# Kernel tuning notes

Measured on AMD Instinct MI355X. Metric: run time of the kernel, lower is better.

The kernel has to match this reference:

```python
import jax, jax.numpy as jnp
import numpy as np

VOCAB = 32000
DEMBED = 512


def embed_position(dembed):
    # Faithful to the torch code: ep[1::2] = ep[0::2]; ep = 1/10000**(ep/dembed);
    # pos = arange(dembed) * ep; odd -> cos, even -> sin.
    i = jnp.arange(dembed, dtype=jnp.float32)
    ep_idx = jnp.floor(i / 2.0) * 2.0           # even index duplicated to the following odd slot
    ep = 1.0 / jnp.power(10000.0, ep_idx / dembed)
    pos = i * ep
    is_odd = (jnp.arange(dembed) % 2) == 1
    return jnp.where(is_odd, jnp.cos(pos), jnp.sin(pos))  # [dembed]


def setup_inputs() -> dict:
    key = jax.random.key(0)
    k1, k2 = jax.random.split(key)
    x = jax.random.randint(k1, (64, 1024), 0, VOCAB, dtype=jnp.int64)
    table = jax.random.normal(k2, (VOCAB, DEMBED), dtype=jnp.float32)
    return {"x": x, "table": table}


def reference(x, table):
    # one-hot matmul == direct gather; fuse with positional add
    pos = embed_position(table.shape[1])         # [dembed]
    return table[x] + pos                        # [B, S, dembed]
```

## Files before the change

kernel.cpp:

```cpp
#include <hip/hip_runtime.h>
#include <hip/hip_bf16.h>
#include <math.h>

#define DEMBED 512
#define NTOK   (64 * 1024)
#define TPB    256
#define BLOCKS 2048
#define STRIDE (BLOCKS * TPB)
#define N4     (NTOK * (DEMBED / 4))
#define ITERS  (N4 / STRIDE)

typedef float f4 __attribute__((ext_vector_type(4)));

__global__ void __launch_bounds__(TPB)
embed_kernel(const int* __restrict__ x,
             const float* __restrict__ table,
             float* __restrict__ out)
{
    const int tid = blockIdx.x * TPB + threadIdx.x;
    const int d4  = tid & 127;

    f4 p;
    const float kLog = logf(10000.0f) / (float)DEMBED;
#pragma unroll
    for (int j = 0; j < 4; ++j) {
        int   i      = d4 * 4 + j;
        float ep_idx = (float)(i & ~1);
        float ep     = expf(-ep_idx * kLog);
        float ang    = (float)i * ep;
        p[j] = (i & 1) ? cosf(ang) : sinf(ang);
    }

    const f4* __restrict__ t4 = (const f4*)table;
    f4*       __restrict__ o4 = (f4*)out;

#pragma unroll
    for (int it = 0; it < ITERS; ++it) {
        int gid = tid + it * STRIDE;
        int tok = gid >> 7;
        int row = x[tok];
        f4  t   = t4[(size_t)row * 128 + d4];
        f4  r   = t + p;
        __builtin_nontemporal_store(r, &o4[gid]);
    }
}

extern "C" void kernel_launch(void* const* d_in, const int* in_sizes, int n_in,
                              void* d_out, int out_size, void* d_ws, size_t ws_size,
                              hipStream_t stream) {
    const int*   x     = (const int*)d_in[0];
    const float* table = (const float*)d_in[1];
    float*       out   = (float*)d_out;

    embed_kernel<<<BLOCKS, TPB, 0, stream>>>(x, table, out);
}
```

Before: 48.39 us.

## Bucket-sort tokens by table row range before gathering embeddings

Adds a counting-sort preprocessing pipeline (zero, histogram, scan, scatter) that groups tokens into 512 buckets by row index >> 6. The embedding kernel then processes tokens in bucketed order and writes each output row back to its original token position. The aim is better cache locality for table reads, since nearby threads now fetch nearby rows. In exchange it adds four extra kernel launches, contended atomics, and an indirect perm load. Output writes are no longer sequential across the grid.

```diff
diff --git a/kernel.cpp b/kernel.cpp
--- a/kernel.cpp
+++ b/kernel.cpp
@@ -9,11 +9,47 @@
 #define STRIDE (BLOCKS * TPB)
 #define N4     (NTOK * (DEMBED / 4))
 #define ITERS  (N4 / STRIDE)
+#define NBUCK  512
 
 typedef float f4 __attribute__((ext_vector_type(4)));
 
+__global__ void zero_kernel(int* __restrict__ counts) {
+    counts[threadIdx.x] = 0;
+}
+
+__global__ void hist_kernel(const int* __restrict__ x, int* __restrict__ counts) {
+    int t = blockIdx.x * blockDim.x + threadIdx.x;
+    atomicAdd(&counts[x[t] >> 6], 1);
+}
+
+__global__ void scan_kernel(const int* __restrict__ counts, int* __restrict__ cursors) {
+    __shared__ int buf[2][NBUCK];
+    int tid = threadIdx.x;
+    int my  = counts[tid];
+    buf[0][tid] = my;
+    __syncthreads();
+    int src = 0;
+    for (int d = 1; d < NBUCK; d <<= 1) {
+        int v = buf[src][tid];
+        if (tid >= d) v += buf[src][tid - d];
+        buf[src ^ 1][tid] = v;
+        src ^= 1;
+        __syncthreads();
+    }
+    cursors[tid] = buf[src][tid] - my;
+}
+
+__global__ void scatter_kernel(const int* __restrict__ x, int* __restrict__ cursors,
+                               int* __restrict__ perm) {
+    int t = blockIdx.x * blockDim.x + threadIdx.x;
+    int b = x[t] >> 6;
+    int p = atomicAdd(&cursors[b], 1);
+    perm[p] = t;
+}
+
 __global__ void __launch_bounds__(TPB)
 embed_kernel(const int* __restrict__ x,
+             const int* __restrict__ perm,
              const float* __restrict__ table,
              float* __restrict__ out)
 {
@@ -36,12 +72,13 @@
 
 #pragma unroll
     for (int it = 0; it < ITERS; ++it) {
-        int gid = tid + it * STRIDE;
-        int tok = gid >> 7;
-        int row = x[tok];
-        f4  t   = t4[(size_t)row * 128 + d4];
-        f4  r   = t + p;
-        __builtin_nontemporal_store(r, &o4[gid]);
+        int gid  = tid + it * STRIDE;
+        int slot = gid >> 7;
+        int tok  = perm[slot];
+        int row  = x[tok];
+        f4  t    = t4[(size_t)row * 128 + d4];
+        f4  r    = t + p;
+        __builtin_nontemporal_store(r, &o4[(size_t)tok * 128 + d4]);
     }
 }
 
@@ -52,5 +89,13 @@
     const float* table = (const float*)d_in[1];
     float*       out   = (float*)d_out;
 
-    embed_kernel<<<BLOCKS, TPB, 0, stream>>>(x, table, out);
+    int* counts  = (int*)d_ws;
+    int* cursors = counts + NBUCK;
+    int* perm    = cursors + NBUCK;
+
+    zero_kernel   <<<1, NBUCK, 0, stream>>>(counts);
+    hist_kernel   <<<NTOK / TPB, TPB, 0, stream>>>(x, counts);
+    scan_kernel   <<<1, NBUCK, 0, stream>>>(counts, cursors);
+    scatter_kernel<<<NTOK / TPB, TPB, 0, stream>>>(x, cursors, perm);
+    embed_kernel  <<<BLOCKS, TPB, 0, stream>>>(x, perm, table, out);
 }
```

Result: slower. 93.90 us (+94.1%).

## Assign contiguous tokens per wavefront with wave-uniform scalar index loads

Applied to the files above, without the earlier changes.

Work is remapped so each 64-lane wavefront handles a contiguous run of tokens (8 per wave), with each lane loading two float4 chunks per row. The wave index is made uniform through readfirstlane, so the token indices can be read with scalar loads up front instead of per-lane redundant loads of x. Each lane now keeps two positional-encoding vectors, which adds a few registers and some setup work. The intent is to cut redundant index-load traffic and address arithmetic in this bandwidth-bound gather.

```diff
diff --git a/kernel.cpp b/kernel.cpp
--- a/kernel.cpp
+++ b/kernel.cpp
@@ -6,9 +6,8 @@
 #define NTOK   (64 * 1024)
 #define TPB    256
 #define BLOCKS 2048
-#define STRIDE (BLOCKS * TPB)
-#define N4     (NTOK * (DEMBED / 4))
-#define ITERS  (N4 / STRIDE)
+#define WAVES  (BLOCKS * TPB / 64)
+#define TPW    (NTOK / WAVES)
 
 typedef float f4 __attribute__((ext_vector_type(4)));
 
@@ -17,31 +16,40 @@
              const float* __restrict__ table,
              float* __restrict__ out)
 {
-    const int tid = blockIdx.x * TPB + threadIdx.x;
-    const int d4  = tid & 127;
+    const int lane = threadIdx.x & 63;
+    int wave = (blockIdx.x * TPB + threadIdx.x) >> 6;
+    wave = __builtin_amdgcn_readfirstlane(wave);
+    const int tok0 = wave * TPW;
 
-    f4 p;
+    f4 pA, pB;
     const float kLog = logf(10000.0f) / (float)DEMBED;
 #pragma unroll
     for (int j = 0; j < 4; ++j) {
-        int   i      = d4 * 4 + j;
-        float ep_idx = (float)(i & ~1);
-        float ep     = expf(-ep_idx * kLog);
-        float ang    = (float)i * ep;
-        p[j] = (i & 1) ? cosf(ang) : sinf(ang);
+        int   ia  = lane * 4 + j;
+        float ea  = expf(-(float)(ia & ~1) * kLog);
+        float aa  = (float)ia * ea;
+        pA[j] = (ia & 1) ? cosf(aa) : sinf(aa);
+        int   ib  = 256 + lane * 4 + j;
+        float eb  = expf(-(float)(ib & ~1) * kLog);
+        float ab  = (float)ib * eb;
+        pB[j] = (ib & 1) ? cosf(ab) : sinf(ab);
     }
 
-    const f4* __restrict__ t4 = (const f4*)table;
-    f4*       __restrict__ o4 = (f4*)out;
+    int rows[TPW];
+#pragma unroll
+    for (int i = 0; i < TPW; ++i)
+        rows[i] = x[tok0 + i];
 
 #pragma unroll
-    for (int it = 0; it < ITERS; ++it) {
-        int gid = tid + it * STRIDE;
-        int tok = gid >> 7;
-        int row = x[tok];
-        f4  t   = t4[(size_t)row * 128 + d4];
-        f4  r   = t + p;
-        __builtin_nontemporal_store(r, &o4[gid]);
+    for (int i = 0; i < TPW; ++i) {
+        const f4* __restrict__ src = (const f4*)(table + (size_t)rows[i] * DEMBED);
+        f4 a = src[lane];
+        f4 b = src[lane + 64];
+        f4 ra = a + pA;
+        f4 rb = b + pB;
+        f4* __restrict__ dst = (f4*)(out + (size_t)(tok0 + i) * DEMBED);
+        __builtin_nontemporal_store(ra, &dst[lane]);
+        __builtin_nontemporal_store(rb, &dst[lane + 64]);
     }
 }
 
```

New measurement: 44.21 us (median of 2 runs). -8.6%, faster.
